# Optimization experiments

Measured on AMD Instinct MI355X. Metric: run time of the kernel, lower is better.

## Reference

```python
import jax, jax.numpy as jnp
import numpy as np


def setup_inputs() -> dict:
    key = jax.random.key(0)
    k1, k2 = jax.random.split(key)
    B, IN, OUT = 1024, 512, 256
    m = jax.random.uniform(k1, (B, IN), dtype=jnp.float32)       # fuzzy memberships in [0,1]
    weight = jax.random.normal(k2, (IN, OUT), dtype=jnp.float32)  # raw weights, clamped in forward
    return {"m": m, "weight": weight}


def reference(m, weight):
    # wf = clamp(weight, 0, 1)
    w = jnp.clip(weight, 0.0, 1.0)
    # min_max: out[b, o] = max_i min(m[b, i], w[i, o])  (tropical-style matmul)
    # broadcast [B, IN, 1] vs [1, IN, OUT] -> min -> max over IN
    inter = jnp.minimum(m[:, :, None], w[None, :, :])  # [B, IN, OUT]
    return jnp.max(inter, axis=1)                       # [B, OUT]
```

## Files before the change

kernel.cpp:

```cpp
#include <hip/hip_runtime.h>


constexpr int IN  = 512;
constexpr int OUT = 256;
constexpr int RPB = 4;
constexpr int G   = 4;
constexpr int KT  = IN / G;

__device__ __forceinline__ float clamp01(float x) {
  return fminf(fmaxf(x, 0.0f), 1.0f);
}

struct W8 { float4 k0,k1,k2,k3,k4,k5,k6,k7; };
struct M8 { float4 lo, hi; };

__device__ __forceinline__ M8 load_m(const float* __restrict__ pm, int k) {
  M8 r;
  r.lo = *reinterpret_cast<const float4*>(pm + k);
  r.hi = *reinterpret_cast<const float4*>(pm + k + 4);
  return r;
}

__device__ __forceinline__ W8 load_w(const float* __restrict__ pw, int k) {
  W8 r;
  r.k0 = *reinterpret_cast<const float4*>(pw + (size_t)(k + 0) * OUT);
  r.k1 = *reinterpret_cast<const float4*>(pw + (size_t)(k + 1) * OUT);
  r.k2 = *reinterpret_cast<const float4*>(pw + (size_t)(k + 2) * OUT);
  r.k3 = *reinterpret_cast<const float4*>(pw + (size_t)(k + 3) * OUT);
  r.k4 = *reinterpret_cast<const float4*>(pw + (size_t)(k + 4) * OUT);
  r.k5 = *reinterpret_cast<const float4*>(pw + (size_t)(k + 5) * OUT);
  r.k6 = *reinterpret_cast<const float4*>(pw + (size_t)(k + 6) * OUT);
  r.k7 = *reinterpret_cast<const float4*>(pw + (size_t)(k + 7) * OUT);
  return r;
}

__device__ __forceinline__ void comp(const M8& mm, const W8& ww, float4& acc) {
  float4 cw;
#define STEP(WV, MV)                          \
  cw.x = clamp01((WV).x); cw.y = clamp01((WV).y); \
  cw.z = clamp01((WV).z); cw.w = clamp01((WV).w); \
  acc.x = fmaxf(acc.x, fminf((MV), cw.x));    \
  acc.y = fmaxf(acc.y, fminf((MV), cw.y));    \
  acc.z = fmaxf(acc.z, fminf((MV), cw.z));    \
  acc.w = fmaxf(acc.w, fminf((MV), cw.w));
  STEP(ww.k0, mm.lo.x)
  STEP(ww.k1, mm.lo.y)
  STEP(ww.k2, mm.lo.z)
  STEP(ww.k3, mm.lo.w)
  STEP(ww.k4, mm.hi.x)
  STEP(ww.k5, mm.hi.y)
  STEP(ww.k6, mm.hi.z)
  STEP(ww.k7, mm.hi.w)
#undef STEP
}

__global__ __launch_bounds__(1024, 4)
void minmax_kernel(const float* __restrict__ m,
                   const float* __restrict__ w,
                   float* __restrict__ out) {
  __shared__ float part[G][RPB][OUT];

  const int tid = threadIdx.x;
  const int cg  = tid & 63;
  const int r   = (tid >> 6) & 3;
  const int ksg = tid >> 8;
  const int c0  = cg * 4;
  const int row = blockIdx.x * RPB + r;

  const float* pm = m + (size_t)row * IN + ksg * KT;
  const float* pw = w + (size_t)(ksg * KT) * OUT + c0;

  float4 acc = make_float4(0.f, 0.f, 0.f, 0.f);

  M8 mA = load_m(pm, 0);
  W8 wA = load_w(pw, 0);
  M8 mB; W8 wB;

#pragma unroll 1
  for (int k = 0; k < KT - 16; k += 16) {
    mB = load_m(pm, k + 8);
    wB = load_w(pw, k + 8);
    comp(mA, wA, acc);
    mA = load_m(pm, k + 16);
    wA = load_w(pw, k + 16);
    comp(mB, wB, acc);
  }
  mB = load_m(pm, KT - 8);
  wB = load_w(pw, KT - 8);
  comp(mA, wA, acc);
  comp(mB, wB, acc);

  *reinterpret_cast<float4*>(&part[ksg][r][c0]) = acc;
  __syncthreads();

  const int rr = tid >> 8;
  const int cc = tid & 255;
  const float v0 = part[0][rr][cc];
  const float v1 = part[1][rr][cc];
  const float v2 = part[2][rr][cc];
  const float v3 = part[3][rr][cc];
  out[(size_t)(blockIdx.x * RPB + rr) * OUT + cc] =
      fmaxf(fmaxf(v0, v1), fmaxf(v2, v3));
}

extern "C" void kernel_launch(void* const* d_in, const int* in_sizes, int n_in,
                              void* d_out, int out_size, void* d_ws, size_t ws_size,
                              hipStream_t stream) {
  (void)n_in; (void)out_size; (void)d_ws; (void)ws_size;
  const float* m = (const float*)d_in[0];
  const float* w = (const float*)d_in[1];
  float* out = (float*)d_out;
  const int B = in_sizes[0] / IN;
  dim3 grid(B / RPB);
  minmax_kernel<<<grid, 1024, 0, stream>>>(m, w, out);
}
```

Baseline: 76.02 us.

## Register-tile four rows per thread to reuse clamped weights across rows

Each thread now accumulates four batch rows for its four output columns, so every loaded and clamped weight vector is reused four times instead of once. The k dimension is split into eight groups with 512-thread blocks, and the shared-memory reduction is widened to eight partials using float2 accesses. This reduces global/L1 weight traffic and clamp instructions per min/max op, at the cost of more registers per thread and fewer resident threads overall.

Result: faster. 66.32 us (-12.8%).

```diff
diff --git a/kernel.cpp b/kernel.cpp
--- a/kernel.cpp
+++ b/kernel.cpp
@@ -4,20 +4,29 @@
 constexpr int IN  = 512;
 constexpr int OUT = 256;
 constexpr int RPB = 4;
-constexpr int G   = 4;
+constexpr int G   = 8;
 constexpr int KT  = IN / G;
 
 __device__ __forceinline__ float clamp01(float x) {
   return fminf(fmaxf(x, 0.0f), 1.0f);
 }
 
-struct W8 { float4 k0,k1,k2,k3,k4,k5,k6,k7; };
-struct M8 { float4 lo, hi; };
+struct W8   { float4 k0,k1,k2,k3,k4,k5,k6,k7; };
+struct M8x4 { float4 r0lo,r0hi,r1lo,r1hi,r2lo,r2hi,r3lo,r3hi; };
 
-__device__ __forceinline__ M8 load_m(const float* __restrict__ pm, int k) {
-  M8 r;
-  r.lo = *reinterpret_cast<const float4*>(pm + k);
-  r.hi = *reinterpret_cast<const float4*>(pm + k + 4);
+__device__ __forceinline__ M8x4 load_m(const float* __restrict__ p0,
+                                       const float* __restrict__ p1,
+                                       const float* __restrict__ p2,
+                                       const float* __restrict__ p3, int k) {
+  M8x4 r;
+  r.r0lo = *reinterpret_cast<const float4*>(p0 + k);
+  r.r0hi = *reinterpret_cast<const float4*>(p0 + k + 4);
+  r.r1lo = *reinterpret_cast<const float4*>(p1 + k);
+  r.r1hi = *reinterpret_cast<const float4*>(p1 + k + 4);
+  r.r2lo = *reinterpret_cast<const float4*>(p2 + k);
+  r.r2hi = *reinterpret_cast<const float4*>(p2 + k + 4);
+  r.r3lo = *reinterpret_cast<const float4*>(p3 + k);
+  r.r3hi = *reinterpret_cast<const float4*>(p3 + k + 4);
   return r;
 }
 
@@ -34,73 +43,85 @@
   return r;
 }
 
-__device__ __forceinline__ void comp(const M8& mm, const W8& ww, float4& acc) {
-  float4 cw;
-#define STEP(WV, MV)                          \
-  cw.x = clamp01((WV).x); cw.y = clamp01((WV).y); \
-  cw.z = clamp01((WV).z); cw.w = clamp01((WV).w); \
-  acc.x = fmaxf(acc.x, fminf((MV), cw.x));    \
-  acc.y = fmaxf(acc.y, fminf((MV), cw.y));    \
-  acc.z = fmaxf(acc.z, fminf((MV), cw.z));    \
-  acc.w = fmaxf(acc.w, fminf((MV), cw.w));
-  STEP(ww.k0, mm.lo.x)
-  STEP(ww.k1, mm.lo.y)
-  STEP(ww.k2, mm.lo.z)
-  STEP(ww.k3, mm.lo.w)
-  STEP(ww.k4, mm.hi.x)
-  STEP(ww.k5, mm.hi.y)
-  STEP(ww.k6, mm.hi.z)
-  STEP(ww.k7, mm.hi.w)
-#undef STEP
+__device__ __forceinline__ void upd(float4& acc, float mv, const float4& cw) {
+  acc.x = fmaxf(acc.x, fminf(mv, cw.x));
+  acc.y = fmaxf(acc.y, fminf(mv, cw.y));
+  acc.z = fmaxf(acc.z, fminf(mv, cw.z));
+  acc.w = fmaxf(acc.w, fminf(mv, cw.w));
 }
 
-__global__ __launch_bounds__(1024, 4)
+__device__ __forceinline__ void comp(const M8x4& mm, const W8& ww,
+                                     float4& a0, float4& a1, float4& a2, float4& a3) {
+  float4 cw;
+#define STEPK(WV, M0, M1, M2, M3)                                   \
+  cw.x = clamp01((WV).x); cw.y = clamp01((WV).y);                   \
+  cw.z = clamp01((WV).z); cw.w = clamp01((WV).w);                   \
+  upd(a0, (M0), cw); upd(a1, (M1), cw); upd(a2, (M2), cw); upd(a3, (M3), cw);
+  STEPK(ww.k0, mm.r0lo.x, mm.r1lo.x, mm.r2lo.x, mm.r3lo.x)
+  STEPK(ww.k1, mm.r0lo.y, mm.r1lo.y, mm.r2lo.y, mm.r3lo.y)
+  STEPK(ww.k2, mm.r0lo.z, mm.r1lo.z, mm.r2lo.z, mm.r3lo.z)
+  STEPK(ww.k3, mm.r0lo.w, mm.r1lo.w, mm.r2lo.w, mm.r3lo.w)
+  STEPK(ww.k4, mm.r0hi.x, mm.r1hi.x, mm.r2hi.x, mm.r3hi.x)
+  STEPK(ww.k5, mm.r0hi.y, mm.r1hi.y, mm.r2hi.y, mm.r3hi.y)
+  STEPK(ww.k6, mm.r0hi.z, mm.r1hi.z, mm.r2hi.z, mm.r3hi.z)
+  STEPK(ww.k7, mm.r0hi.w, mm.r1hi.w, mm.r2hi.w, mm.r3hi.w)
+#undef STEPK
+}
+
+__global__ __launch_bounds__(512, 2)
 void minmax_kernel(const float* __restrict__ m,
                    const float* __restrict__ w,
                    float* __restrict__ out) {
   __shared__ float part[G][RPB][OUT];
 
-  const int tid = threadIdx.x;
-  const int cg  = tid & 63;
-  const int r   = (tid >> 6) & 3;
-  const int ksg = tid >> 8;
-  const int c0  = cg * 4;
-  const int row = blockIdx.x * RPB + r;
+  const int tid  = threadIdx.x;
+  const int cg   = tid & 63;
+  const int ksg  = tid >> 6;
+  const int c0   = cg * 4;
+  const int row0 = blockIdx.x * RPB;
 
-  const float* pm = m + (size_t)row * IN + ksg * KT;
-  const float* pw = w + (size_t)(ksg * KT) * OUT + c0;
+  const float* pm0 = m + (size_t)row0 * IN + ksg * KT;
+  const float* pm1 = pm0 + IN;
+  const float* pm2 = pm1 + IN;
+  const float* pm3 = pm2 + IN;
+  const float* pw  = w + (size_t)(ksg * KT) * OUT + c0;
 
-  float4 acc = make_float4(0.f, 0.f, 0.f, 0.f);
+  float4 a0 = make_float4(0.f,0.f,0.f,0.f);
+  float4 a1 = a0, a2 = a0, a3 = a0;
 
-  M8 mA = load_m(pm, 0);
-  W8 wA = load_w(pw, 0);
-  M8 mB; W8 wB;
+  M8x4 mA = load_m(pm0, pm1, pm2, pm3, 0);
+  W8   wA = load_w(pw, 0);
+  M8x4 mB; W8 wB;
 
 #pragma unroll 1
   for (int k = 0; k < KT - 16; k += 16) {
-    mB = load_m(pm, k + 8);
+    mB = load_m(pm0, pm1, pm2, pm3, k + 8);
     wB = load_w(pw, k + 8);
-    comp(mA, wA, acc);
-    mA = load_m(pm, k + 16);
+    comp(mA, wA, a0, a1, a2, a3);
+    mA = load_m(pm0, pm1, pm2, pm3, k + 16);
     wA = load_w(pw, k + 16);
-    comp(mB, wB, acc);
+    comp(mB, wB, a0, a1, a2, a3);
   }
-  mB = load_m(pm, KT - 8);
+  mB = load_m(pm0, pm1, pm2, pm3, KT - 8);
   wB = load_w(pw, KT - 8);
-  comp(mA, wA, acc);
-  comp(mB, wB, acc);
+  comp(mA, wA, a0, a1, a2, a3);
+  comp(mB, wB, a0, a1, a2, a3);
 
-  *reinterpret_cast<float4*>(&part[ksg][r][c0]) = acc;
+  *reinterpret_cast<float4*>(&part[ksg][0][c0]) = a0;
+  *reinterpret_cast<float4*>(&part[ksg][1][c0]) = a1;
+  *reinterpret_cast<float4*>(&part[ksg][2][c0]) = a2;
+  *reinterpret_cast<float4*>(&part[ksg][3][c0]) = a3;
   __syncthreads();
 
-  const int rr = tid >> 8;
-  const int cc = tid & 255;
-  const float v0 = part[0][rr][cc];
-  const float v1 = part[1][rr][cc];
-  const float v2 = part[2][rr][cc];
-  const float v3 = part[3][rr][cc];
-  out[(size_t)(blockIdx.x * RPB + rr) * OUT + cc] =
-      fmaxf(fmaxf(v0, v1), fmaxf(v2, v3));
+  const int o  = tid * 2;
+  const int rr = o >> 8;
+  const int cc = o & 255;
+  float2 v = *reinterpret_cast<const float2*>(&part[0][rr][cc]);
+#define RED(g) { float2 t = *reinterpret_cast<const float2*>(&part[(g)][rr][cc]); \
+                 v.x = fmaxf(v.x, t.x); v.y = fmaxf(v.y, t.y); }
+  RED(1) RED(2) RED(3) RED(4) RED(5) RED(6) RED(7)
+#undef RED
+  *reinterpret_cast<float2*>(&out[(size_t)(row0 + rr) * OUT + cc]) = v;
 }
 
 extern "C" void kernel_launch(void* const* d_in, const int* in_sizes, int n_in,
@@ -112,5 +133,5 @@
   float* out = (float*)d_out;
   const int B = in_sizes[0] / IN;
   dim3 grid(B / RPB);
-  minmax_kernel<<<grid, 1024, 0, stream>>>(m, w, out);
+  minmax_kernel<<<grid, 512, 0, stream>>>(m, w, out);
 }
```
